# Kernel tuning notes

Measured on AMD Instinct MI355X. Metric: run time of the kernel, lower is better.

Reference implementation:

```python
import jax, jax.numpy as jnp
import numpy as np

N_NODES = 50000
N_EDGES = 800000
HID = 128
N_PROC = 3  # num_layers - 1 processor iterations (shared weights)


def _mlp(x, w1, b1, w2, b2, w3, b3):
    h = jax.nn.relu(x @ w1 + b1)
    h = jax.nn.relu(h @ w2 + b2)
    return h @ w3 + b3


def setup_inputs() -> dict:
    key = jax.random.key(0)
    ks = jax.random.split(key, 32)

    def p(k, shape):
        fan_in = shape[0]
        return (jax.random.normal(k, shape, dtype=jnp.float32) / np.float32(np.sqrt(fan_in)))

    inp = {
        "X_curr": jax.random.normal(ks[0], (N_NODES, 6), dtype=jnp.float32),
        "y_prev": jax.random.normal(ks[1], (N_NODES,), dtype=jnp.float32),
        "edge": jax.random.randint(ks[2], (2, N_EDGES), 0, N_NODES, dtype=jnp.int32),
        "mode": 0,
        # EdgeModel net: Linear(9,H) ReLU Linear(H,H) ReLU Linear(H,3)
        "ew1": p(ks[3], (9, HID)), "eb1": jnp.zeros((HID,), jnp.float32),
        "ew2": p(ks[4], (HID, HID)), "eb2": jnp.zeros((HID,), jnp.float32),
        "ew3": p(ks[5], (HID, 3)), "eb3": jnp.zeros((3,), jnp.float32),
        # NodeModel net: Linear(5,H) ReLU Linear(H,H) ReLU Linear(H,1)
        "nw1": p(ks[6], (5, HID)), "nb1": jnp.zeros((HID,), jnp.float32),
        "nw2": p(ks[7], (HID, HID)), "nb2": jnp.zeros((HID,), jnp.float32),
        "nw3": p(ks[8], (HID, 1)), "nb3": jnp.zeros((1,), jnp.float32),
        # decoder: Linear(5,H) ReLU Linear(H,H) ReLU Linear(H,H) ReLU Linear(H,1)
        "dw1": p(ks[9], (5, HID)), "db1": jnp.zeros((HID,), jnp.float32),
        "dw2": p(ks[10], (HID, HID)), "db2": jnp.zeros((HID,), jnp.float32),
        "dw3": p(ks[11], (HID, HID)), "db3": jnp.zeros((HID,), jnp.float32),
        "dw4": p(ks[12], (HID, 1)), "db4": jnp.zeros((1,), jnp.float32),
    }
    return inp


def reference(X_curr, y_prev,
              ew1, eb1, ew2, eb2, ew3, eb3,
              nw1, nb1, nw2, nb2, nw3, nb3,
              dw1, db1, dw2, db2, dw3, db3, dw4, db4,
              edge, mode):
    n = X_curr.shape[0]
    src_idx, dst_idx = edge[0], edge[1]
    # x_in = cat(X_curr[:, [0,1,2,4]], y_prev)  -> [N, 5]
    x = jnp.concatenate([X_curr[:, jnp.array([0, 1, 2, 4])], y_prev[:, None]], axis=-1)

    # _compute_edge_attr: grad_r = (f_dest - f_src) * disp_r
    xs, xd = x[src_idx], x[dst_idx]
    disp = xd[:, :3] - xs[:, :3]
    edge_attr = (xd[:, 4] - xs[:, 4])[:, None] * disp  # [E, 3]

    # degree for scatter-mean (nodes with no incoming edges aggregate to 0)
    deg = jax.ops.segment_sum(jnp.ones((edge.shape[1],), x.dtype), dst_idx, num_segments=n)
    inv_deg = jnp.where(deg > 0, 1.0 / jnp.maximum(deg, 1.0), 0.0)

    for _ in range(N_PROC):
        # EdgeModel
        xs, xd = x[src_idx], x[dst_idx]
        disp = xd[:, :3] - xs[:, :3]
        norm_r = jnp.linalg.norm(disp, axis=-1, keepdims=True)
        net_in = jnp.concatenate([disp, norm_r, edge_attr, xs[:, 4:5], xd[:, 4:5]], axis=-1)  # [E, 9]
        edge_attr = edge_attr + _mlp(net_in, ew1, eb1, ew2, eb2, ew3, eb3)
        # NodeModel: message = edge_attr, aggr='mean' at target (edge[1])
        aggr = jax.ops.segment_sum(edge_attr, dst_idx, num_segments=n) * inv_deg[:, None]  # [N, 3]
        node_in = jnp.concatenate([x[:, 3:5], aggr], axis=-1)  # [N, 5]
        delta = _mlp(node_in, nw1, nb1, nw2, nb2, nw3, nb3)[:, 0]
        x = x.at[:, 4].add(delta)

    # decoder
    h = jax.nn.relu(x @ dw1 + db1)
    h = jax.nn.relu(h @ dw2 + db2)
    h = jax.nn.relu(h @ dw3 + db3)
    x_out = h @ dw4 + db4  # [N, 1]
    return y_prev + x_out[:, 0]
```

## Files before the change

kernel.cpp:

```cpp
#include <hip/hip_runtime.h>

typedef float f32x4 __attribute__((ext_vector_type(4)));
typedef __bf16 bf16x8 __attribute__((ext_vector_type(8)));
typedef __bf16 bf16x4 __attribute__((ext_vector_type(4)));

#define WB_W1E 0
#define WB_W2E 4096
#define WB_W3E 20480
#define WB_W1N 22528
#define WB_W2N 26624
#define WB_W3N 43008
#define WB_W1D 45056
#define WB_W2D 49152
#define WB_W3D 65536
#define WB_W4D 81920
#define WB_TOTAL 83968

#define BKT_SHIFT 6
#define BKT_SZ 64

__global__ void k_prep(const float* __restrict__ ew1, const float* __restrict__ eb1,
                       const float* __restrict__ ew2, const float* __restrict__ ew3,
                       const float* __restrict__ nw1, const float* __restrict__ nb1,
                       const float* __restrict__ nw2, const float* __restrict__ nw3,
                       const float* __restrict__ dw1, const float* __restrict__ db1,
                       const float* __restrict__ dw2, const float* __restrict__ dw3,
                       const float* __restrict__ dw4, __bf16* __restrict__ wb) {
  int gid = blockIdx.x * 256 + threadIdx.x;
  if (gid >= WB_TOTAL) return;
  const float* srcs[10] = {ew1, ew2, ew3, nw1, nw2, nw3, dw1, dw2, dw3, dw4};
  const float* brow[10] = {eb1, 0, 0, nb1, 0, 0, db1, 0, 0, 0};
  const int Ks[10] = {9, 128, 128, 5, 128, 128, 5, 128, 128, 128};
  const int Ns[10] = {128, 128, 3, 128, 128, 1, 128, 128, 128, 1};
  const int CTs[10] = {8, 8, 1, 8, 8, 1, 8, 8, 8, 1};
  const int cum[11] = {0, 4096, 20480, 22528, 26624, 43008, 45056, 49152, 65536, 81920, 83968};
  int seg = 0;
  while (gid >= cum[seg + 1]) seg++;
  int li = gid - cum[seg];
  int j = li & 7;
  int lane = (li >> 3) & 63;
  int fi = li >> 9;
  int CT = CTs[seg];
  int ct = fi % CT;
  int kt = fi / CT;
  int k = kt * 32 + ((lane >> 4) << 3) + j;
  int n = ct * 16 + (lane & 15);
  int kl;
  if (seg == 0) {
    if (k < 4) kl = k;
    else if (k >= 8 && k < 13) kl = k - 4;
    else kl = (k == 13) ? -2 : -1;
  } else if (seg == 3 || seg == 6) {
    if (k < 5) kl = k;
    else kl = (k == 5) ? -2 : -1;
  } else {
    kl = (k < Ks[seg]) ? k : -1;
  }
  float v = 0.f;
  if (n < Ns[seg]) {
    if (kl >= 0) v = srcs[seg][kl * Ns[seg] + n];
    else if (kl == -2 && brow[seg]) v = brow[seg][n];
  }
  wb[gid] = (__bf16)v;
}

__global__ void k_zero(const float* __restrict__ y_prev, float* __restrict__ x4,
                       int* __restrict__ bcnt, int n, int nbkt) {
  int i = blockIdx.x * 256 + threadIdx.x;
  if (i < n) x4[i] = y_prev[i];
  if (i <= nbkt) bcnt[i] = 0;
}

__global__ __launch_bounds__(256) void k_cntb(const int* __restrict__ dstp,
                                              int* __restrict__ bcnt, int nbkt, int E) {
  __shared__ int hist[1024];
  int tid = threadIdx.x;
  for (int t = tid; t < nbkt; t += 256) hist[t] = 0;
  __syncthreads();
  int e0 = blockIdx.x * 8192;
#pragma unroll
  for (int j = 0; j < 32; j++) {
    int e = e0 + j * 256 + tid;
    if (e < E) atomicAdd(&hist[dstp[e] >> BKT_SHIFT], 1);
  }
  __syncthreads();
  for (int t = tid; t < nbkt; t += 256) {
    int c = hist[t];
    if (c) atomicAdd(&bcnt[t], c);
  }
}

__global__ void k_scanb(const int* __restrict__ bcnt, int* __restrict__ bstart,
                        int* __restrict__ cur, int* __restrict__ rp, int nbkt, int n, int E) {
  __shared__ int sd[1024];
  int t = threadIdx.x;
  int c = (t < nbkt) ? bcnt[t] : 0;
  sd[t] = c;
  __syncthreads();
#pragma unroll
  for (int off = 1; off < 1024; off <<= 1) {
    int v = sd[t];
    int u = (t >= off) ? sd[t - off] : 0;
    __syncthreads();
    sd[t] = v + u;
    __syncthreads();
  }
  if (t < nbkt) {
    int ex = sd[t] - c;
    bstart[t] = ex;
    cur[t] = ex;
  }
  if (t == 0) {
    bstart[nbkt] = E;
    rp[n] = E;
  }
}

__global__ __launch_bounds__(256) void k_bin(const int* __restrict__ dstp, int* __restrict__ cur,
                                             int* __restrict__ eix, int nbkt, int E) {
  __shared__ int hist[1024];
  __shared__ int base[1024];
  int tid = threadIdx.x;
  for (int t = tid; t < nbkt; t += 256) hist[t] = 0;
  __syncthreads();
  int e0 = blockIdx.x * 8192;
  int b[32], lr[32];
#pragma unroll
  for (int j = 0; j < 32; j++) {
    int e = e0 + j * 256 + tid;
    if (e < E) {
      b[j] = dstp[e] >> BKT_SHIFT;
      lr[j] = atomicAdd(&hist[b[j]], 1);
    } else {
      b[j] = -1;
      lr[j] = 0;
    }
  }
  __syncthreads();
  for (int t = tid; t < nbkt; t += 256) {
    int c = hist[t];
    base[t] = c ? atomicAdd(&cur[t], c) : 0;
  }
  __syncthreads();
#pragma unroll
  for (int j = 0; j < 32; j++)
    if (b[j] >= 0) eix[base[b[j]] + lr[j]] = e0 + j * 256 + tid;
}

__global__ __launch_bounds__(256) void k_build(const int* __restrict__ srcO,
                                               const int* __restrict__ dstO,
                                               const float* __restrict__ Xc,
                                               const float* __restrict__ yp,
                                               const int* __restrict__ bstart, const int* eix,
                                               int* __restrict__ srcS, int* dstS,
                                               float* __restrict__ peS, float* __restrict__ eaS,
                                               int* __restrict__ rp, float* __restrict__ invdeg,
                                               int n) {
  __shared__ int cnt[BKT_SZ];
  __shared__ int starts[BKT_SZ];
  int tid = threadIdx.x;
  int d0 = blockIdx.x << BKT_SHIFT;
  if (tid < BKT_SZ) cnt[tid] = 0;
  int gstart = bstart[blockIdx.x], gend = bstart[blockIdx.x + 1];
  __syncthreads();
  int ei[16], dd[16], rr[16];
#pragma unroll
  for (int k = 0; k < 16; k++) {
    int p = gstart + k * 256 + tid;
    ei[k] = (p < gend) ? eix[p] : -1;
  }
#pragma unroll
  for (int k = 0; k < 16; k++) {
    if (ei[k] >= 0) {
      dd[k] = dstO[ei[k]];
      rr[k] = atomicAdd(&cnt[dd[k] - d0], 1);
    }
  }
  __syncthreads();
  if (tid < 64) {
    int c = cnt[tid];
    int s = c;
#pragma unroll
    for (int off = 1; off < 64; off <<= 1) {
      int u = __shfl_up(s, off);
      if (tid >= off) s += u;
    }
    int ex = s - c;
    starts[tid] = ex;
    int d = d0 + tid;
    if (d < n) {
      rp[d] = gstart + ex;
      invdeg[d] = c > 0 ? 1.0f / (float)c : 0.f;
    }
  }
  __syncthreads();
#pragma unroll
  for (int k = 0; k < 16; k++) {
    int e = ei[k];
    if (e < 0) continue;
    int s = srcO[e], d = dd[k];
    float dx = Xc[d * 6 + 0] - Xc[s * 6 + 0];
    float dy = Xc[d * 6 + 1] - Xc[s * 6 + 1];
    float dz = Xc[d * 6 + 2] - Xc[s * 6 + 2];
    float nr = sqrtf(dx * dx + dy * dy + dz * dz);
    float w = yp[d] - yp[s];
    int q = gstart + starts[d - d0] + rr[k];
    srcS[q] = s;
    dstS[q] = d;
    f32x4 pv = {dx, dy, dz, nr};
    *(f32x4*)(peS + 4 * q) = pv;
    f32x4 av = {w * dx, w * dy, w * dz, 0.f};
    *(f32x4*)(eaS + 4 * q) = av;
  }
}

__device__ __forceinline__ int aoff(int row, int b) { return (row * 256 + b) ^ ((row & 7) << 4); }

__device__ __forceinline__ void wg_sync() {
  asm volatile("s_waitcnt lgkmcnt(0)" ::: "memory");
  __builtin_amdgcn_s_barrier();
}

__device__ __forceinline__ bf16x4 relu_pack(f32x4 a) {
  bf16x4 p;
#pragma unroll
  for (int r = 0; r < 4; r++) {
    float v = a[r];
    p[r] = (__bf16)(v > 0.f ? v : 0.f);
  }
  return p;
}

__global__ __attribute__((amdgpu_flat_work_group_size(256, 256), amdgpu_waves_per_eu(3, 4))) void
k_edge(const float* __restrict__ x4, const float* __restrict__ pe, float* __restrict__ ea,
       const int* __restrict__ src, const int* __restrict__ dstp,
       const __bf16* __restrict__ W1f, const __bf16* __restrict__ W2f,
       const __bf16* __restrict__ W3f, const float* __restrict__ b2,
       const float* __restrict__ b3, int ntiles, int E) {
  __shared__ char Ab[16384];
  __shared__ char Bb[16384];
  const int tid = threadIdx.x;
  const int l = tid & 63, w = tid >> 6;
  const int col = l & 15, krow = l >> 4;
  const int rl = w * 16 + (l >> 2), chunk = l & 3;

  bf16x8 w1r[2], w2r[4][2], w3r[4];
#pragma unroll
  for (int t = 0; t < 2; t++) w1r[t] = *(const bf16x8*)(W1f + ((2 * w + t) << 9) + l * 8);
#pragma unroll
  for (int kt = 0; kt < 4; kt++)
#pragma unroll
    for (int t = 0; t < 2; t++)
      w2r[kt][t] = *(const bf16x8*)(W2f + ((kt * 8 + 2 * w + t) << 9) + l * 8);
#pragma unroll
  for (int kt = 0; kt < 4; kt++) w3r[kt] = *(const bf16x8*)(W3f + (kt << 9) + l * 8);
  f32x4 b2c[2];
#pragma unroll
  for (int t = 0; t < 2; t++) b2c[t] = *(const f32x4*)(b2 + (2 * w + t) * 16 + krow * 4);
  f32x4 b3i = {0.f, 0.f, 0.f, 0.f};
  if (krow == 0) {
    b3i[0] = b3[0];
    b3i[1] = b3[1];
    b3i[2] = b3[2];
  }

  int tile = blockIdx.x;
  if (tile >= ntiles) return;

  int e0 = tile * 64 + rl;
  int ec = e0 < E ? e0 : E - 1;
  int cs = src[ec], cd = dstp[ec];
  f32x4 cld = {0.f, 0.f, 0.f, 0.f};
  if (chunk < 2) cld = *(const f32x4*)(((chunk == 1) ? ea : pe) + 4 * ec);
  float cxs = 0.f, cxd = 0.f;
  if (chunk == 1) {
    cxs = x4[cs];
    cxd = x4[cd];
  }

  for (;;) {
    bf16x8 v;
#pragma unroll
    for (int q = 0; q < 8; q++) v[q] = (__bf16)0.f;
    if (chunk == 0) {
      v[0] = (__bf16)cld[0];
      v[1] = (__bf16)cld[1];
      v[2] = (__bf16)cld[2];
      v[3] = (__bf16)cld[3];
    } else if (chunk == 1) {
      v[0] = (__bf16)cld[0];
      v[1] = (__bf16)cld[1];
      v[2] = (__bf16)cld[2];
      v[3] = (__bf16)cxs;
      v[4] = (__bf16)cxd;
      v[5] = (__bf16)1.0f;
    }
    *(bf16x8*)(Ab + aoff(rl, chunk * 16)) = v;

    int nt = tile + (int)gridDim.x;
    bool hn = nt < ntiles;
    int tc = hn ? nt : tile;
    int en = tc * 64 + rl;
    if (en >= E) en = E - 1;
    int ns = src[en], nd = dstp[en];

    wg_sync();

    f32x4 h[4][2];
#pragma unroll
    for (int c = 0; c < 4; c++)
#pragma unroll
      for (int t = 0; t < 2; t++) {
        f32x4 z = {0.f, 0.f, 0.f, 0.f};
        h[c][t] = z;
      }
    bf16x8 bb[4];
#pragma unroll
    for (int c = 0; c < 4; c++) bb[c] = *(const bf16x8*)(Ab + aoff(c * 16 + col, krow * 16));
#pragma unroll
    for (int c = 0; c < 4; c++)
#pragma unroll
      for (int t = 0; t < 2; t++)
        h[c][t] = __builtin_amdgcn_mfma_f32_16x16x32_bf16(w1r[t], bb[c], h[c][t], 0, 0, 0);
#pragma unroll
    for (int c = 0; c < 4; c++)
#pragma unroll
      for (int t = 0; t < 2; t++)
        *(bf16x4*)(Bb + aoff(c * 16 + col, (2 * w + t) * 32 + krow * 8)) = relu_pack(h[c][t]);

    wg_sync();

    f32x4 nld = {0.f, 0.f, 0.f, 0.f};
    if (chunk < 2) nld = *(const f32x4*)(((chunk == 1) ? ea : pe) + 4 * en);
    float nxs = 0.f, nxd = 0.f;
    if (chunk == 1) {
      nxs = x4[ns];
      nxd = x4[nd];
    }

#pragma unroll
    for (int c = 0; c < 4; c++)
#pragma unroll
      for (int t = 0; t < 2; t++) h[c][t] = b2c[t];
#pragma unroll
    for (int kt = 0; kt < 4; kt++) {
#pragma unroll
      for (int c = 0; c < 4; c++)
        bb[c] = *(const bf16x8*)(Bb + aoff(c * 16 + col, kt * 64 + krow * 16));
#pragma unroll
      for (int c = 0; c < 4; c++)
#pragma unroll
        for (int t = 0; t < 2; t++)
          h[c][t] = __builtin_amdgcn_mfma_f32_16x16x32_bf16(w2r[kt][t], bb[c], h[c][t], 0, 0, 0);
    }
#pragma unroll
    for (int c = 0; c < 4; c++)
#pragma unroll
      for (int t = 0; t < 2; t++)
        *(bf16x4*)(Ab + aoff(c * 16 + col, (2 * w + t) * 32 + krow * 8)) = relu_pack(h[c][t]);

    wg_sync();

    f32x4 o = b3i;
#pragma unroll
    for (int kt = 0; kt < 4; kt++) {
      bf16x8 bq = *(const bf16x8*)(Ab + aoff(w * 16 + col, kt * 64 + krow * 16));
      o = __builtin_amdgcn_mfma_f32_16x16x32_bf16(w3r[kt], bq, o, 0, 0, 0);
    }

    if (krow == 0) {
      int e3 = tile * 64 + w * 16 + col;
      if (e3 < E) {
        f32x4 oe = *(const f32x4*)(ea + 4 * e3);
        f32x4 nv;
        nv[0] = oe[0] + o[0];
        nv[1] = oe[1] + o[1];
        nv[2] = oe[2] + o[2];
        nv[3] = 0.f;
        *(f32x4*)(ea + 4 * e3) = nv;
      }
    }

    if (!hn) break;
    tile = nt;
    cld = nld;
    cxs = nxs;
    cxd = nxd;
  }
}

__global__ __attribute__((amdgpu_flat_work_group_size(256, 256), amdgpu_waves_per_eu(3, 4))) void
k_node(float* __restrict__ x4, const float* __restrict__ Xc, const float* __restrict__ eaS,
       const int* __restrict__ rp, const float* __restrict__ invdeg,
       const __bf16* __restrict__ W1f, const __bf16* __restrict__ W2f,
       const __bf16* __restrict__ W3f, const float* __restrict__ b2,
       const float* __restrict__ b3, int n) {
  __shared__ char Ab[16384];
  __shared__ char Bb[16384];
  const int tid = threadIdx.x;
  const int l = tid & 63, w = tid >> 6;
  const int col = l & 15, krow = l >> 4;
  const int rl = w * 16 + (l >> 2), chunk = l & 3;

  bf16x8 w1r[2], w2r[4][2], w3r[4];
#pragma unroll
  for (int t = 0; t < 2; t++) w1r[t] = *(const bf16x8*)(W1f + ((2 * w + t) << 9) + l * 8);
#pragma unroll
  for (int kt = 0; kt < 4; kt++)
#pragma unroll
    for (int t = 0; t < 2; t++)
      w2r[kt][t] = *(const bf16x8*)(W2f + ((kt * 8 + 2 * w + t) << 9) + l * 8);
#pragma unroll
  for (int kt = 0; kt < 4; kt++) w3r[kt] = *(const bf16x8*)(W3f + (kt << 9) + l * 8);
  f32x4 b2c[2];
#pragma unroll
  for (int t = 0; t < 2; t++) b2c[t] = *(const f32x4*)(b2 + (2 * w + t) * 16 + krow * 4);
  float b3s = b3[0];

  int tile = blockIdx.x;
  int i0 = tile * 64 + rl;
  bool vi = i0 < n;
  int i = vi ? i0 : (n - 1);

  int ss = rp[i], se = rp[i + 1];
  float a0 = 0.f, a1 = 0.f, a2 = 0.f;
  for (int p = ss + chunk; p < se; p += 4) {
    f32x4 ev = *(const f32x4*)(eaS + 4 * p);
    a0 += ev[0];
    a1 += ev[1];
    a2 += ev[2];
  }
  a0 += __shfl_xor(a0, 1);
  a1 += __shfl_xor(a1, 1);
  a2 += __shfl_xor(a2, 1);
  a0 += __shfl_xor(a0, 2);
  a1 += __shfl_xor(a1, 2);
  a2 += __shfl_xor(a2, 2);

  bf16x8 v;
#pragma unroll
  for (int q = 0; q < 8; q++) v[q] = (__bf16)0.f;
  if (chunk == 0) {
    float x3 = Xc[i * 6 + 4];
    float xv = x4[i];
    float iv = invdeg[i];
    v[0] = (__bf16)x3;
    v[1] = (__bf16)xv;
    v[2] = (__bf16)(a0 * iv);
    v[3] = (__bf16)(a1 * iv);
    v[4] = (__bf16)(a2 * iv);
    v[5] = (__bf16)1.0f;
  }
  *(bf16x8*)(Ab + aoff(rl, chunk * 16)) = v;

  wg_sync();

  f32x4 h[4][2];
#pragma unroll
  for (int c = 0; c < 4; c++)
#pragma unroll
    for (int t = 0; t < 2; t++) {
      f32x4 z = {0.f, 0.f, 0.f, 0.f};
      h[c][t] = z;
    }
  bf16x8 bb[4];
#pragma unroll
  for (int c = 0; c < 4; c++) bb[c] = *(const bf16x8*)(Ab + aoff(c * 16 + col, krow * 16));
#pragma unroll
  for (int c = 0; c < 4; c++)
#pragma unroll
    for (int t = 0; t < 2; t++)
      h[c][t] = __builtin_amdgcn_mfma_f32_16x16x32_bf16(w1r[t], bb[c], h[c][t], 0, 0, 0);
#pragma unroll
  for (int c = 0; c < 4; c++)
#pragma unroll
    for (int t = 0; t < 2; t++)
      *(bf16x4*)(Bb + aoff(c * 16 + col, (2 * w + t) * 32 + krow * 8)) = relu_pack(h[c][t]);

  wg_sync();

#pragma unroll
  for (int c = 0; c < 4; c++)
#pragma unroll
    for (int t = 0; t < 2; t++) h[c][t] = b2c[t];
#pragma unroll
  for (int kt = 0; kt < 4; kt++) {
#pragma unroll
    for (int c = 0; c < 4; c++)
      bb[c] = *(const bf16x8*)(Bb + aoff(c * 16 + col, kt * 64 + krow * 16));
#pragma unroll
    for (int c = 0; c < 4; c++)
#pragma unroll
      for (int t = 0; t < 2; t++)
        h[c][t] = __builtin_amdgcn_mfma_f32_16x16x32_bf16(w2r[kt][t], bb[c], h[c][t], 0, 0, 0);
  }
#pragma unroll
  for (int c = 0; c < 4; c++)
#pragma unroll
    for (int t = 0; t < 2; t++)
      *(bf16x4*)(Ab + aoff(c * 16 + col, (2 * w + t) * 32 + krow * 8)) = relu_pack(h[c][t]);

  wg_sync();

  f32x4 o = {0.f, 0.f, 0.f, 0.f};
  if (krow == 0) o[0] = b3s;
#pragma unroll
  for (int kt = 0; kt < 4; kt++) {
    bf16x8 bq = *(const bf16x8*)(Ab + aoff(w * 16 + col, kt * 64 + krow * 16));
    o = __builtin_amdgcn_mfma_f32_16x16x32_bf16(w3r[kt], bq, o, 0, 0, 0);
  }

  if (krow == 0) {
    int i3 = tile * 64 + w * 16 + col;
    if (i3 < n) x4[i3] = x4[i3] + o[0];
  }
}

__global__ __attribute__((amdgpu_flat_work_group_size(256, 256), amdgpu_waves_per_eu(2, 4))) void
k_dec(const float* __restrict__ x4, const float* __restrict__ Xc, const float* __restrict__ y_prev,
      const __bf16* __restrict__ W1f, const __bf16* __restrict__ W2f,
      const __bf16* __restrict__ W3f, const __bf16* __restrict__ W4f,
      const float* __restrict__ b2, const float* __restrict__ b3, const float* __restrict__ b4,
      float* __restrict__ out, int n) {
  __shared__ char Ab[16384];
  __shared__ char Bb[16384];
  const int tid = threadIdx.x;
  const int l = tid & 63, w = tid >> 6;
  const int col = l & 15, krow = l >> 4;
  const int rl = w * 16 + (l >> 2), chunk = l & 3;

  bf16x8 w1r[2], w2r[4][2], w3r[4][2], w4r[4];
#pragma unroll
  for (int t = 0; t < 2; t++) w1r[t] = *(const bf16x8*)(W1f + ((2 * w + t) << 9) + l * 8);
#pragma unroll
  for (int kt = 0; kt < 4; kt++)
#pragma unroll
    for (int t = 0; t < 2; t++) {
      w2r[kt][t] = *(const bf16x8*)(W2f + ((kt * 8 + 2 * w + t) << 9) + l * 8);
      w3r[kt][t] = *(const bf16x8*)(W3f + ((kt * 8 + 2 * w + t) << 9) + l * 8);
    }
#pragma unroll
  for (int kt = 0; kt < 4; kt++) w4r[kt] = *(const bf16x8*)(W4f + (kt << 9) + l * 8);
  f32x4 b2c[2], b3c[2];
#pragma unroll
  for (int t = 0; t < 2; t++) {
    b2c[t] = *(const f32x4*)(b2 + (2 * w + t) * 16 + krow * 4);
    b3c[t] = *(const f32x4*)(b3 + (2 * w + t) * 16 + krow * 4);
  }
  float b4s = b4[0];

  int tile = blockIdx.x;
  int i0 = tile * 64 + rl;
  bool vi = i0 < n;
  int i = vi ? i0 : (n - 1);

  bf16x8 v;
#pragma unroll
  for (int q = 0; q < 8; q++) v[q] = (__bf16)0.f;
  if (chunk == 0) {
    v[0] = (__bf16)Xc[i * 6 + 0];
    v[1] = (__bf16)Xc[i * 6 + 1];
    v[2] = (__bf16)Xc[i * 6 + 2];
    v[3] = (__bf16)Xc[i * 6 + 4];
    v[4] = (__bf16)x4[i];
    v[5] = (__bf16)1.0f;
  }
  *(bf16x8*)(Ab + aoff(rl, chunk * 16)) = v;

  wg_sync();

  f32x4 h[4][2];
  bf16x8 bb[4];
#pragma unroll
  for (int c = 0; c < 4; c++)
#pragma unroll
    for (int t = 0; t < 2; t++) {
      f32x4 z = {0.f, 0.f, 0.f, 0.f};
      h[c][t] = z;
    }
#pragma unroll
  for (int c = 0; c < 4; c++) bb[c] = *(const bf16x8*)(Ab + aoff(c * 16 + col, krow * 16));
#pragma unroll
  for (int c = 0; c < 4; c++)
#pragma unroll
    for (int t = 0; t < 2; t++)
      h[c][t] = __builtin_amdgcn_mfma_f32_16x16x32_bf16(w1r[t], bb[c], h[c][t], 0, 0, 0);
#pragma unroll
  for (int c = 0; c < 4; c++)
#pragma unroll
    for (int t = 0; t < 2; t++)
      *(bf16x4*)(Bb + aoff(c * 16 + col, (2 * w + t) * 32 + krow * 8)) = relu_pack(h[c][t]);

  wg_sync();

#pragma unroll
  for (int c = 0; c < 4; c++)
#pragma unroll
    for (int t = 0; t < 2; t++) h[c][t] = b2c[t];
#pragma unroll
  for (int kt = 0; kt < 4; kt++) {
#pragma unroll
    for (int c = 0; c < 4; c++)
      bb[c] = *(const bf16x8*)(Bb + aoff(c * 16 + col, kt * 64 + krow * 16));
#pragma unroll
    for (int c = 0; c < 4; c++)
#pragma unroll
      for (int t = 0; t < 2; t++)
        h[c][t] = __builtin_amdgcn_mfma_f32_16x16x32_bf16(w2r[kt][t], bb[c], h[c][t], 0, 0, 0);
  }
#pragma unroll
  for (int c = 0; c < 4; c++)
#pragma unroll
    for (int t = 0; t < 2; t++)
      *(bf16x4*)(Ab + aoff(c * 16 + col, (2 * w + t) * 32 + krow * 8)) = relu_pack(h[c][t]);

  wg_sync();

#pragma unroll
  for (int c = 0; c < 4; c++)
#pragma unroll
    for (int t = 0; t < 2; t++) h[c][t] = b3c[t];
#pragma unroll
  for (int kt = 0; kt < 4; kt++) {
#pragma unroll
    for (int c = 0; c < 4; c++)
      bb[c] = *(const bf16x8*)(Ab + aoff(c * 16 + col, kt * 64 + krow * 16));
#pragma unroll
    for (int c = 0; c < 4; c++)
#pragma unroll
      for (int t = 0; t < 2; t++)
        h[c][t] = __builtin_amdgcn_mfma_f32_16x16x32_bf16(w3r[kt][t], bb[c], h[c][t], 0, 0, 0);
  }
#pragma unroll
  for (int c = 0; c < 4; c++)
#pragma unroll
    for (int t = 0; t < 2; t++)
      *(bf16x4*)(Bb + aoff(c * 16 + col, (2 * w + t) * 32 + krow * 8)) = relu_pack(h[c][t]);

  wg_sync();

  f32x4 o = {0.f, 0.f, 0.f, 0.f};
  if (krow == 0) o[0] = b4s;
#pragma unroll
  for (int kt = 0; kt < 4; kt++) {
    bf16x8 bq = *(const bf16x8*)(Bb + aoff(w * 16 + col, kt * 64 + krow * 16));
    o = __builtin_amdgcn_mfma_f32_16x16x32_bf16(w4r[kt], bq, o, 0, 0, 0);
  }

  if (krow == 0) {
    int i3 = tile * 64 + w * 16 + col;
    if (i3 < n) out[i3] = y_prev[i3] + o[0];
  }
}

extern "C" void kernel_launch(void* const* d_in, const int* in_sizes, int n_in, void* d_out,
                              int out_size, void* d_ws, size_t ws_size, hipStream_t stream) {
  const float* Xc = (const float*)d_in[0];
  const float* y_prev = (const float*)d_in[1];
  const int* edge = (const int*)d_in[2];
  const float* ew1 = (const float*)d_in[4];
  const float* eb1 = (const float*)d_in[5];
  const float* ew2 = (const float*)d_in[6];
  const float* eb2 = (const float*)d_in[7];
  const float* ew3 = (const float*)d_in[8];
  const float* eb3 = (const float*)d_in[9];
  const float* nw1 = (const float*)d_in[10];
  const float* nb1 = (const float*)d_in[11];
  const float* nw2 = (const float*)d_in[12];
  const float* nb2 = (const float*)d_in[13];
  const float* nw3 = (const float*)d_in[14];
  const float* nb3 = (const float*)d_in[15];
  const float* dw1 = (const float*)d_in[16];
  const float* db1 = (const float*)d_in[17];
  const float* dw2 = (const float*)d_in[18];
  const float* db2 = (const float*)d_in[19];
  const float* dw3 = (const float*)d_in[20];
  const float* db3 = (const float*)d_in[21];
  const float* dw4 = (const float*)d_in[22];
  const float* db4 = (const float*)d_in[23];

  int n = in_sizes[0] / 6;
  int E = in_sizes[2] / 2;
  const int* srcp = edge;
  const int* dstp = edge + E;

  __bf16* wb = (__bf16*)d_ws;
  float* fbase = (float*)((char*)d_ws + (size_t)WB_TOTAL * 2);
  size_t na = ((size_t)n + 3) & ~(size_t)3;
  float* x4 = fbase;
  float* invdeg = fbase + na;
  int* rp = (int*)(fbase + 2 * na);
  int* bcnt = rp + na + 8;
  int* bstart = bcnt + 1056;
  int* cur = bstart + 1056;
  int* srcS = cur + 1024;
  int* dstS = srcS + E;
  float* peS = (float*)(dstS + E);
  float* eaS = peS + 4 * (size_t)E;

  size_t need = (size_t)WB_TOTAL * 2 + (3 * na + 8 + 3136 + 10 * (size_t)E) * 4;
  if (ws_size < need) return;

  dim3 B(256);
  int nblk = (n + 255) / 256;
  int nbkt = (n + BKT_SZ - 1) / BKT_SZ;
  int eblk = (E + 8191) / 8192;
  k_prep<<<dim3((WB_TOTAL + 255) / 256), B, 0, stream>>>(ew1, eb1, ew2, ew3, nw1, nb1, nw2, nw3,
                                                         dw1, db1, dw2, dw3, dw4, wb);
  k_zero<<<dim3(nblk), B, 0, stream>>>(y_prev, x4, bcnt, n, nbkt);
  k_cntb<<<dim3(eblk), B, 0, stream>>>(dstp, bcnt, nbkt, E);
  k_scanb<<<dim3(1), dim3(1024), 0, stream>>>(bcnt, bstart, cur, rp, nbkt, n, E);
  k_bin<<<dim3(eblk), B, 0, stream>>>(dstp, cur, dstS, nbkt, E);
  k_build<<<dim3(nbkt), B, 0, stream>>>(srcp, dstp, Xc, y_prev, bstart, dstS, srcS, dstS, peS,
                                        eaS, rp, invdeg, n);

  int etiles = (E + 63) / 64;
  int vtiles = (n + 63) / 64;
  int egrid = etiles < 768 ? etiles : 768;
  for (int it = 0; it < 3; it++) {
    k_edge<<<dim3(egrid), B, 0, stream>>>(x4, peS, eaS, srcS, dstS, wb + WB_W1E, wb + WB_W2E,
                                          wb + WB_W3E, eb2, eb3, etiles, E);
    k_node<<<dim3(vtiles), B, 0, stream>>>(x4, Xc, eaS, rp, invdeg, wb + WB_W1N, wb + WB_W2N,
                                           wb + WB_W3N, nb2, nb3, n);
  }
  k_dec<<<dim3(vtiles), B, 0, stream>>>(x4, Xc, y_prev, wb + WB_W1D, wb + WB_W2D, wb + WB_W3D,
                                        wb + WB_W4D, db2, db3, db4, (float*)d_out, n);
}
```

Measured before the change: 253.6 us.

## Split edge MLP work per wave as 2x2 edge/neuron tiles and widen LDS swizzle

Each wave in the edge MLP kernel now computes half the edge tile across half the hidden neurons (2x4 MFMA blocks), instead of all 64 edges across a quarter of the neurons. Each wave therefore reads half as many activation fragments from LDS per MFMA and holds twice as many weight registers. To fit the larger register footprint, the minimum waves-per-EU hint drops from 3 to 2, and the LDS XOR swizzle now uses 16 row phases instead of 8 to reduce bank conflicts. The risk is lower occupancy from the extra weight registers, which may hurt latency hiding for the gather loads.

```diff
diff --git a/kernel.cpp b/kernel.cpp
--- a/kernel.cpp
+++ b/kernel.cpp
@@ -214,7 +214,7 @@
   }
 }
 
-__device__ __forceinline__ int aoff(int row, int b) { return (row * 256 + b) ^ ((row & 7) << 4); }
+__device__ __forceinline__ int aoff(int row, int b) { return (row * 256 + b) ^ ((row & 15) << 4); }
 
 __device__ __forceinline__ void wg_sync() {
   asm volatile("s_waitcnt lgkmcnt(0)" ::: "memory");
@@ -231,7 +231,7 @@
   return p;
 }
 
-__global__ __attribute__((amdgpu_flat_work_group_size(256, 256), amdgpu_waves_per_eu(3, 4))) void
+__global__ __attribute__((amdgpu_flat_work_group_size(256, 256), amdgpu_waves_per_eu(2, 4))) void
 k_edge(const float* __restrict__ x4, const float* __restrict__ pe, float* __restrict__ ea,
        const int* __restrict__ src, const int* __restrict__ dstp,
        const __bf16* __restrict__ W1f, const __bf16* __restrict__ W2f,
@@ -243,20 +243,21 @@
   const int l = tid & 63, w = tid >> 6;
   const int col = l & 15, krow = l >> 4;
   const int rl = w * 16 + (l >> 2), chunk = l & 3;
-
-  bf16x8 w1r[2], w2r[4][2], w3r[4];
-#pragma unroll
-  for (int t = 0; t < 2; t++) w1r[t] = *(const bf16x8*)(W1f + ((2 * w + t) << 9) + l * 8);
+  const int eh = w & 1, nh = w >> 1;
+
+  bf16x8 w1r[4], w2r[4][4], w3r[4];
+#pragma unroll
+  for (int tt = 0; tt < 4; tt++) w1r[tt] = *(const bf16x8*)(W1f + ((nh * 4 + tt) << 9) + l * 8);
 #pragma unroll
   for (int kt = 0; kt < 4; kt++)
 #pragma unroll
-    for (int t = 0; t < 2; t++)
-      w2r[kt][t] = *(const bf16x8*)(W2f + ((kt * 8 + 2 * w + t) << 9) + l * 8);
+    for (int tt = 0; tt < 4; tt++)
+      w2r[kt][tt] = *(const bf16x8*)(W2f + ((kt * 8 + nh * 4 + tt) << 9) + l * 8);
 #pragma unroll
   for (int kt = 0; kt < 4; kt++) w3r[kt] = *(const bf16x8*)(W3f + (kt << 9) + l * 8);
-  f32x4 b2c[2];
-#pragma unroll
-  for (int t = 0; t < 2; t++) b2c[t] = *(const f32x4*)(b2 + (2 * w + t) * 16 + krow * 4);
+  f32x4 b2c[4];
+#pragma unroll
+  for (int tt = 0; tt < 4; tt++) b2c[tt] = *(const f32x4*)(b2 + nh * 64 + tt * 16 + krow * 4);
   f32x4 b3i = {0.f, 0.f, 0.f, 0.f};
   if (krow == 0) {
     b3i[0] = b3[0];
@@ -306,27 +307,24 @@
 
     wg_sync();
 
-    f32x4 h[4][2];
-#pragma unroll
-    for (int c = 0; c < 4; c++)
-#pragma unroll
-      for (int t = 0; t < 2; t++) {
+    f32x4 h[2][4];
+    bf16x8 bb[2];
+#pragma unroll
+    for (int c2 = 0; c2 < 2; c2++)
+      bb[c2] = *(const bf16x8*)(Ab + aoff((eh * 2 + c2) * 16 + col, krow * 16));
+#pragma unroll
+    for (int c2 = 0; c2 < 2; c2++)
+#pragma unroll
+      for (int tt = 0; tt < 4; tt++) {
         f32x4 z = {0.f, 0.f, 0.f, 0.f};
-        h[c][t] = z;
+        h[c2][tt] = __builtin_amdgcn_mfma_f32_16x16x32_bf16(w1r[tt], bb[c2], z, 0, 0, 0);
       }
-    bf16x8 bb[4];
-#pragma unroll
-    for (int c = 0; c < 4; c++) bb[c] = *(const bf16x8*)(Ab + aoff(c * 16 + col, krow * 16));
-#pragma unroll
-    for (int c = 0; c < 4; c++)
-#pragma unroll
-      for (int t = 0; t < 2; t++)
-        h[c][t] = __builtin_amdgcn_mfma_f32_16x16x32_bf16(w1r[t], bb[c], h[c][t], 0, 0, 0);
-#pragma unroll
-    for (int c = 0; c < 4; c++)
-#pragma unroll
-      for (int t = 0; t < 2; t++)
-        *(bf16x4*)(Bb + aoff(c * 16 + col, (2 * w + t) * 32 + krow * 8)) = relu_pack(h[c][t]);
+#pragma unroll
+    for (int c2 = 0; c2 < 2; c2++)
+#pragma unroll
+      for (int tt = 0; tt < 4; tt++)
+        *(bf16x4*)(Bb + aoff((eh * 2 + c2) * 16 + col, nh * 128 + tt * 32 + krow * 8)) =
+            relu_pack(h[c2][tt]);
 
     wg_sync();
 
@@ -339,25 +337,27 @@
     }
 
 #pragma unroll
-    for (int c = 0; c < 4; c++)
-#pragma unroll
-      for (int t = 0; t < 2; t++) h[c][t] = b2c[t];
+    for (int c2 = 0; c2 < 2; c2++)
+#pragma unroll
+      for (int tt = 0; tt < 4; tt++) h[c2][tt] = b2c[tt];
 #pragma unroll
     for (int kt = 0; kt < 4; kt++) {
 #pragma unroll
-      for (int c = 0; c < 4; c++)
-        bb[c] = *(const bf16x8*)(Bb + aoff(c * 16 + col, kt * 64 + krow * 16));
-#pragma unroll
-      for (int c = 0; c < 4; c++)
-#pragma unroll
-        for (int t = 0; t < 2; t++)
-          h[c][t] = __builtin_amdgcn_mfma_f32_16x16x32_bf16(w2r[kt][t], bb[c], h[c][t], 0, 0, 0);
-    }
-#pragma unroll
-    for (int c = 0; c < 4; c++)
-#pragma unroll
-      for (int t = 0; t < 2; t++)
-        *(bf16x4*)(Ab + aoff(c * 16 + col, (2 * w + t) * 32 + krow * 8)) = relu_pack(h[c][t]);
+      for (int c2 = 0; c2 < 2; c2++)
+        bb[c2] = *(const bf16x8*)(Bb + aoff(eh * 32 + c2 * 16 + col, kt * 64 + krow * 16));
+#pragma unroll
+      for (int c2 = 0; c2 < 2; c2++)
+#pragma unroll
+        for (int tt = 0; tt < 4; tt++)
+          h[c2][tt] = __builtin_amdgcn_mfma_f32_16x16x32_bf16(w2r[kt][tt], bb[c2], h[c2][tt], 0,
+                                                              0, 0);
+    }
+#pragma unroll
+    for (int c2 = 0; c2 < 2; c2++)
+#pragma unroll
+      for (int tt = 0; tt < 4; tt++)
+        *(bf16x4*)(Ab + aoff(eh * 32 + c2 * 16 + col, nh * 128 + tt * 32 + krow * 8)) =
+            relu_pack(h[c2][tt]);
 
     wg_sync();
 
```

Result: slower. 296.4 us (+16.9%).
